# Kernel tuning notes

Hardware: AMD Instinct MI355X
Metric: run time of the kernel (lower is better)

Reference implementation:

```python
import jax, jax.numpy as jnp
import numpy as np

N_NODES = 100000
N_EDGES = 3200000
NEG_SLOPE = 0.2  # PyG GATConv default


def _gat_conv(x, src, dst, W, a_src, a_dst, b, num_nodes):
    # x: [N, Fin]; src/dst: [E'] (self-loops already appended)
    h = x @ W                                   # [N, Fout]
    alpha_src = h @ a_src                       # [N]
    alpha_dst = h @ a_dst                       # [N]
    e = jax.nn.leaky_relu(alpha_src[src] + alpha_dst[dst], NEG_SLOPE)  # [E']
    # segment softmax over incoming edges of each destination node
    e_max = jax.ops.segment_max(e, dst, num_segments=num_nodes)
    e_exp = jnp.exp(e - e_max[dst])
    denom = jax.ops.segment_sum(e_exp, dst, num_segments=num_nodes)
    alpha = e_exp / (denom[dst] + 1e-16)        # [E']
    out = jax.ops.segment_sum(h[src] * alpha[:, None], dst, num_segments=num_nodes)
    return out + b


def setup_inputs() -> dict:
    key = jax.random.key(0)
    ks = jax.random.split(key, 10)
    x = jax.random.normal(ks[0], (N_NODES, 1), jnp.float32)
    edge_index = jax.random.randint(ks[1], (2, N_EDGES), 0, N_NODES, dtype=jnp.int64)
    s1 = 1.0  # glorot-ish scales
    return {
        "x": x,
        "edge_index": edge_index,
        "W1": jax.random.normal(ks[2], (1, 20), jnp.float32) * s1,
        "a_src1": jax.random.normal(ks[3], (20,), jnp.float32) * 0.3,
        "a_dst1": jax.random.normal(ks[4], (20,), jnp.float32) * 0.3,
        "b1": jnp.zeros((20,), jnp.float32),
        "W2": jax.random.normal(ks[5], (20, 20), jnp.float32) * (1.0 / np.sqrt(20.0)),
        "a_src2": jax.random.normal(ks[6], (20,), jnp.float32) * 0.3,
        "a_dst2": jax.random.normal(ks[7], (20,), jnp.float32) * 0.3,
        "b2": jnp.zeros((20,), jnp.float32),
        "Wl": jax.random.normal(ks[8], (20, 1), jnp.float32) * (1.0 / np.sqrt(20.0)),
        "bl": jnp.zeros((1,), jnp.float32),
    }


def reference(x, edge_index, W1, a_src1, a_dst1, b1, W2, a_src2, a_dst2, b2, Wl, bl):
    n = x.shape[0]
    loop = jnp.arange(n, dtype=edge_index.dtype)
    src = jnp.concatenate([edge_index[0], loop])  # add_self_loops=True
    dst = jnp.concatenate([edge_index[1], loop])
    h = _gat_conv(x, src, dst, W1, a_src1, a_dst1, b1, n)
    h = jax.nn.relu(h)
    h = _gat_conv(h, src, dst, W2, a_src2, a_dst2, b2, n)
    h = jax.nn.relu(h)
    return h @ Wl + bl  # [N, 1]
```

## Files before the change

### kernel.cpp

```cpp
#include <hip/hip_runtime.h>
#include <hip/hip_fp16.h>

#define FDIM 20
#define NSLOPE 0.2f
#define BSHIFT 7
#define BSIZE 128
#define BCAP 4800
#define MAXBUCK 800
#define PGRID 512
#define HSTRIDE 32
#define ABLK 512
#define ITMAX 7
#define CHCAP 6272
#define OFFSTRIDE 132

__device__ __forceinline__ float lrelu(float v) { return v > 0.f ? v : NSLOPE * v; }

__global__ void __launch_bounds__(1024)
k_part(const int* __restrict__ ei, int E, int nbuck,
       const float* __restrict__ x, const float* __restrict__ W1,
       const float* __restrict__ a_src, const float* __restrict__ a_dst,
       float2* __restrict__ PX, float* __restrict__ AD,
       int* __restrict__ gcur, int* __restrict__ slab, int N)
{
    __shared__ int hist[MAXBUCK];
    __shared__ int lofs[MAXBUCK];
    __shared__ int gbase[MAXBUCK];
    __shared__ int sbuf[CHCAP];
    __shared__ unsigned short sbk[CHCAP];
    const int tid = threadIdx.x;

    {
        int g = blockIdx.x * 1024 + tid;
        if (g < N) {
            float cs = 0.f, cd = 0.f;
#pragma unroll
            for (int f = 0; f < FDIM; ++f) {
                float w = W1[f]; cs += w * a_src[f]; cd += w * a_dst[f];
            }
            float xv = x[g];
            PX[g] = make_float2(xv * cs, xv);
            AD[g] = xv * cd;
        }
    }

    const int chunk = (E + PGRID - 1) / PGRID;
    const int c0 = blockIdx.x * chunk;
    const int c1 = min(c0 + chunk, E);
    for (int t = tid; t < nbuck; t += 1024) hist[t] = 0;
    __syncthreads();

    int ent[ITMAX], meta[ITMAX];
#pragma unroll
    for (int it = 0; it < ITMAX; ++it) {
        int i = c0 + tid + (it << 10);
        meta[it] = -1;
        if (i < c1) {
            int s = ei[i], d = ei[E + i];
            int b = d >> BSHIFT;
            int lp = atomicAdd(&hist[b], 1);
            ent[it]  = (s << BSHIFT) | (d & (BSIZE - 1));
            meta[it] = (lp << 10) | b;
        }
    }
    __syncthreads();

    int myc = 0;
    if (tid < nbuck) {
        myc = hist[tid];
        lofs[tid] = myc;
        gbase[tid] = myc ? atomicAdd(gcur + tid, myc) : 0;
    }
    __syncthreads();
    for (int o = 1; o < nbuck; o <<= 1) {
        int v = 0;
        if (tid < nbuck && tid >= o) v = lofs[tid - o];
        __syncthreads();
        if (tid < nbuck && tid >= o) lofs[tid] += v;
        __syncthreads();
    }
    if (tid < nbuck) lofs[tid] -= myc;
    __syncthreads();

#pragma unroll
    for (int it = 0; it < ITMAX; ++it) {
        int m = meta[it];
        if (m >= 0) {
            int b  = m & 1023;
            int lp = m >> 10;
            int pos = lofs[b] + lp;
            sbuf[pos] = ent[it];
            sbk[pos]  = (unsigned short)b;
        }
    }
    __syncthreads();

    const int cnt = c1 - c0;
    for (int i = tid; i < cnt; i += 1024) {
        int b  = sbk[i];
        int gp = gbase[b] + (i - lofs[b]);
        if (gp < BCAP) slab[(size_t)b * BCAP + gp] = sbuf[i];
    }
}

__device__ __forceinline__ void sort_bucket(const int* __restrict__ sp, int cnt,
                                            int* __restrict__ sedge,
                                            int* __restrict__ off,
                                            int* __restrict__ cur)
{
    const int tid = threadIdx.x;
    if (tid < BSIZE + 1) off[tid] = 0;
    __syncthreads();
    for (int i = tid; i < cnt; i += ABLK)
        atomicAdd(&off[(sp[i] & (BSIZE - 1)) + 1], 1);
    __syncthreads();
    if (tid < 64) {
        int a = off[2 * tid + 1];
        int c = off[2 * tid + 2];
        int s = a + c;
#pragma unroll
        for (int o = 1; o < 64; o <<= 1) {
            int t = __shfl_up(s, o);
            if (tid >= o) s += t;
        }
        int ex = s - a - c;
        off[2 * tid]     = ex;
        off[2 * tid + 1] = ex + a;
        cur[2 * tid]     = ex;
        cur[2 * tid + 1] = ex + a;
        if (tid == 63) off[BSIZE] = s;
    }
    __syncthreads();
    for (int i = tid; i < cnt; i += ABLK) {
        int e = sp[i];
        int pos = atomicAdd(&cur[e & (BSIZE - 1)], 1);
        sedge[pos] = e >> BSHIFT;
    }
    __syncthreads();
}

__global__ void __launch_bounds__(ABLK)
k_agg1(const int* __restrict__ gcur, const int* __restrict__ slab,
       const float2* __restrict__ PX, const float* __restrict__ AD,
       const float* __restrict__ W1, const float* __restrict__ b1,
       const float* __restrict__ W2,
       const float* __restrict__ as2w, const float* __restrict__ ad2w,
       __half* __restrict__ H, float* __restrict__ AD2,
       int* __restrict__ sedge_g, int* __restrict__ off_g, int N)
{
    __shared__ int sedge[BCAP];
    __shared__ int off[BSIZE + 1], cur[BSIZE];
    __shared__ float sAD[BSIZE];
    __shared__ float sW1[FDIM], sb1[FDIM], sW2[FDIM * FDIM], sas[FDIM], sad[FDIM];
    const int tid = threadIdx.x;
    const int b = blockIdx.x;
    const int dbase = b << BSHIFT;
    if (tid < BSIZE) { int d = dbase + tid; sAD[tid] = (d < N) ? AD[d] : 0.f; }
    for (int t = tid; t < FDIM * FDIM; t += ABLK) sW2[t] = W2[t];
    if (tid >= 480 && tid < 480 + FDIM) {
        int k = tid - 480;
        sW1[k] = W1[k]; sb1[k] = b1[k]; sas[k] = as2w[k]; sad[k] = ad2w[k];
    }
    const int cnt = min(gcur[b], BCAP);
    sort_bucket(slab + (size_t)b * BCAP, cnt, sedge, off, cur);

    for (int i = tid; i < cnt; i += ABLK) sedge_g[(size_t)b * BCAP + i] = sedge[i];
    if (tid <= BSIZE) off_g[b * OFFSTRIDE + tid] = off[tid];

    const int dl = tid >> 2, sub = tid & 3;
    const float adv = sAD[dl];
    float den = 0.f, sx = 0.f;
    const int e1 = off[dl + 1];
#pragma unroll 2
    for (int j = off[dl] + sub; j < e1; j += 4) {
        int s = sedge[j];
        float2 p = PX[s];
        float w = __expf(lrelu(p.x + adv));
        den += w; sx += w * p.y;
    }
    den += __shfl_xor(den, 1); den += __shfl_xor(den, 2);
    sx  += __shfl_xor(sx, 1);  sx  += __shfl_xor(sx, 2);
    const int d = dbase + dl;
    if (sub == 0 && d < N) {
        float2 p = PX[d];
        float w = __expf(lrelu(p.x + adv));
        den += w; sx += w * p.y;
        float sv = sx / (den + 1e-16f);
        float tk[FDIM];
#pragma unroll
        for (int k = 0; k < FDIM; ++k) {
            float tv = sv * sW1[k] + sb1[k];
            tk[k] = tv > 0.f ? tv : 0.f;
        }
        float pas = 0.f, pad = 0.f;
        __half2* hrow = (__half2*)(H + (size_t)d * HSTRIDE);
#pragma unroll
        for (int f = 0; f < FDIM; f += 2) {
            float h0 = 0.f, h1 = 0.f;
#pragma unroll
            for (int k = 0; k < FDIM; ++k) {
                h0 += tk[k] * sW2[k * FDIM + f];
                h1 += tk[k] * sW2[k * FDIM + f + 1];
            }
            hrow[f >> 1] = __halves2half2(__float2half(h0), __float2half(h1));
            pas += h0 * sas[f] + h1 * sas[f + 1];
            pad += h0 * sad[f] + h1 * sad[f + 1];
        }
        *(float*)(H + (size_t)d * HSTRIDE + 24) = pas;
        AD2[d] = pad;
    }
}

__global__ void __launch_bounds__(ABLK)
k_agg2(const int* __restrict__ gcur, const int* __restrict__ sedge_g,
       const int* __restrict__ off_g,
       const __half* __restrict__ H, const float* __restrict__ AD2,
       const float* __restrict__ b2, const float* __restrict__ Wl,
       const float* __restrict__ bl,
       float* __restrict__ out, int N)
{
    __shared__ int sedge[BCAP];
    __shared__ int off[BSIZE + 1];
    __shared__ float sAD[BSIZE];
    __shared__ float sb2[FDIM], sWl[FDIM];
    const int tid = threadIdx.x;
    const int b = blockIdx.x;
    const int dbase = b << BSHIFT;
    if (tid < BSIZE) { int d = dbase + tid; sAD[tid] = (d < N) ? AD2[d] : 0.f; }
    if (tid >= 480 && tid < 480 + FDIM) {
        int k = tid - 480;
        sb2[k] = b2[k]; sWl[k] = Wl[k];
    }
    const int cnt = min(gcur[b], BCAP);
    for (int i = tid; i < cnt; i += ABLK) sedge[i] = sedge_g[(size_t)b * BCAP + i];
    if (tid <= BSIZE) off[tid] = off_g[b * OFFSTRIDE + tid];
    __syncthreads();

    const int dl = tid >> 2, sub = tid & 3;
    const int lane3 = (tid & 63) | 3;
    const float adv = sAD[dl];
    float den = 0.f;
    float acc[8];
#pragma unroll
    for (int t = 0; t < 8; ++t) acc[t] = 0.f;
    const int e1 = off[dl + 1];
#pragma unroll 2
    for (int j = off[dl]; j < e1; ++j) {
        int s = sedge[j];
        uint4 q = ((const uint4*)(H + (size_t)s * HSTRIDE))[sub];
        float al = __shfl(__uint_as_float(q.x), lane3);
        float w = __expf(lrelu(al + adv));
        den += w;
        float2 f;
        f = __half22float2(*(__half2*)&q.x); acc[0] += w * f.x; acc[1] += w * f.y;
        f = __half22float2(*(__half2*)&q.y); acc[2] += w * f.x; acc[3] += w * f.y;
        f = __half22float2(*(__half2*)&q.z); acc[4] += w * f.x; acc[5] += w * f.y;
        f = __half22float2(*(__half2*)&q.w); acc[6] += w * f.x; acc[7] += w * f.y;
    }

    const int d = dbase + dl;
    float r = 0.f;
    if (d < N) {
        uint4 q = ((const uint4*)(H + (size_t)d * HSTRIDE))[sub];
        float al = __shfl(__uint_as_float(q.x), lane3);
        float w = __expf(lrelu(al + adv));
        den += w;
        float hv[8];
        float2 f;
        f = __half22float2(*(__half2*)&q.x); hv[0] = f.x; hv[1] = f.y;
        f = __half22float2(*(__half2*)&q.y); hv[2] = f.x; hv[3] = f.y;
        f = __half22float2(*(__half2*)&q.z); hv[4] = f.x; hv[5] = f.y;
        f = __half22float2(*(__half2*)&q.w); hv[6] = f.x; hv[7] = f.y;
        float inv = 1.f / (den + 1e-16f);
        const int base = sub << 3;
        const int nf = (sub < 2) ? 8 : (sub == 2 ? 4 : 0);
#pragma unroll
        for (int t = 0; t < 8; ++t) {
            if (t < nf) {
                float v = (acc[t] + w * hv[t]) * inv + sb2[base + t];
                v = v > 0.f ? v : 0.f;
                r += v * sWl[base + t];
            }
        }
    }
    r += __shfl_xor(r, 1);
    r += __shfl_xor(r, 2);
    if (sub == 0 && d < N) out[d] = r + bl[0];
}

extern "C" void kernel_launch(void* const* d_in, const int* in_sizes, int n_in,
                              void* d_out, int out_size, void* d_ws, size_t ws_size,
                              hipStream_t stream)
{
    const float* x      = (const float*)d_in[0];
    const int*   ei     = (const int*)d_in[1];
    const float* W1     = (const float*)d_in[2];
    const float* a_src1 = (const float*)d_in[3];
    const float* a_dst1 = (const float*)d_in[4];
    const float* b1     = (const float*)d_in[5];
    const float* W2     = (const float*)d_in[6];
    const float* a_src2 = (const float*)d_in[7];
    const float* a_dst2 = (const float*)d_in[8];
    const float* b2     = (const float*)d_in[9];
    const float* Wl     = (const float*)d_in[10];
    const float* bl     = (const float*)d_in[11];
    float* out = (float*)d_out;

    const int N = in_sizes[0];
    const int E = in_sizes[1] / 2;
    const int NBUCK = (N + BSIZE - 1) >> BSHIFT;

    __half* H    = (__half*)d_ws;
    float2* PX   = (float2*)(H + (size_t)N * HSTRIDE);
    float*  AD   = (float*)(PX + N);
    float*  AD2  = AD + N;
    int*  gcur   = (int*)(AD2 + N);
    int*  slab   = gcur + MAXBUCK;
    int*  sedge_g = slab + (size_t)MAXBUCK * BCAP;
    int*  off_g   = sedge_g + (size_t)MAXBUCK * BCAP;

    hipMemsetAsync(gcur, 0, MAXBUCK * sizeof(int), stream);
    k_part<<<PGRID, 1024, 0, stream>>>(ei, E, NBUCK, x, W1, a_src1, a_dst1,
                                       PX, AD, gcur, slab, N);
    k_agg1<<<NBUCK, ABLK, 0, stream>>>(gcur, slab, PX, AD, W1, b1, W2,
                                       a_src2, a_dst2, H, AD2, sedge_g, off_g, N);
    k_agg2<<<NBUCK, ABLK, 0, stream>>>(gcur, sedge_g, off_g, H, AD2, b2, Wl, bl, out, N);
}
```

Measured before the change: 183.8 us.

## Split agg2 edges across sub-lanes and spread layer-2 transform across four lanes

In the second aggregation kernel, each of the four lanes per destination now handles a quarter of the edges and loads the full 48-byte H row. Before, all four lanes walked every edge and each read its own 16-byte slice. Partial sums for the 20 features and the denominator are then reduced with shuffles. In the first aggregation kernel, the per-node 20x20 W2 transform and the H row store are now split over the four sub-lanes, which were idle before. The first-layer edge loop unroll is also raised to 4. The trade-off is more registers (20 accumulators) and more shuffle reductions, in exchange for fewer serial edge iterations per lane.

```diff
diff --git a/kernel.cpp b/kernel.cpp
--- a/kernel.cpp
+++ b/kernel.cpp
@@ -171,7 +171,7 @@
     const float adv = sAD[dl];
     float den = 0.f, sx = 0.f;
     const int e1 = off[dl + 1];
-#pragma unroll 2
+#pragma unroll 4
     for (int j = off[dl] + sub; j < e1; j += 4) {
         int s = sedge[j];
         float2 p = PX[s];
@@ -181,7 +181,7 @@
     den += __shfl_xor(den, 1); den += __shfl_xor(den, 2);
     sx  += __shfl_xor(sx, 1);  sx  += __shfl_xor(sx, 2);
     const int d = dbase + dl;
-    if (sub == 0 && d < N) {
+    if (d < N) {
         float2 p = PX[d];
         float w = __expf(lrelu(p.x + adv));
         den += w; sx += w * p.y;
@@ -192,22 +192,34 @@
             float tv = sv * sW1[k] + sb1[k];
             tk[k] = tv > 0.f ? tv : 0.f;
         }
+        const int fbase = sub << 3;
+        const int nf = (sub < 2) ? 8 : (sub == 2 ? 4 : 0);
+        float hv[8];
         float pas = 0.f, pad = 0.f;
-        __half2* hrow = (__half2*)(H + (size_t)d * HSTRIDE);
-#pragma unroll
-        for (int f = 0; f < FDIM; f += 2) {
-            float h0 = 0.f, h1 = 0.f;
-#pragma unroll
-            for (int k = 0; k < FDIM; ++k) {
-                h0 += tk[k] * sW2[k * FDIM + f];
-                h1 += tk[k] * sW2[k * FDIM + f + 1];
+#pragma unroll
+        for (int t = 0; t < 8; ++t) {
+            float hsum = 0.f;
+            if (t < nf) {
+#pragma unroll
+                for (int k = 0; k < FDIM; ++k)
+                    hsum += tk[k] * sW2[k * FDIM + fbase + t];
+                pas += hsum * sas[fbase + t];
+                pad += hsum * sad[fbase + t];
             }
-            hrow[f >> 1] = __halves2half2(__float2half(h0), __float2half(h1));
-            pas += h0 * sas[f] + h1 * sas[f + 1];
-            pad += h0 * sad[f] + h1 * sad[f + 1];
-        }
-        *(float*)(H + (size_t)d * HSTRIDE + 24) = pas;
-        AD2[d] = pad;
+            hv[t] = hsum;
+        }
+        pas += __shfl_xor(pas, 1); pas += __shfl_xor(pas, 2);
+        pad += __shfl_xor(pad, 1); pad += __shfl_xor(pad, 2);
+        __half2 p01 = __halves2half2(__float2half(hv[0]), __float2half(hv[1]));
+        __half2 p23 = __halves2half2(__float2half(hv[2]), __float2half(hv[3]));
+        __half2 p45 = __halves2half2(__float2half(hv[4]), __float2half(hv[5]));
+        __half2 p67 = __halves2half2(__float2half(hv[6]), __float2half(hv[7]));
+        uint4 q;
+        q.x = *(unsigned*)&p01; q.y = *(unsigned*)&p23;
+        q.z = *(unsigned*)&p45; q.w = *(unsigned*)&p67;
+        if (sub == 2) { q.z = __float_as_uint(pas); q.w = 0u; }
+        if (sub < 3) ((uint4*)(H + (size_t)d * HSTRIDE))[sub] = q;
+        else AD2[d] = pad;
     }
 }
 
@@ -237,55 +249,67 @@
     __syncthreads();
 
     const int dl = tid >> 2, sub = tid & 3;
-    const int lane3 = (tid & 63) | 3;
     const float adv = sAD[dl];
     float den = 0.f;
-    float acc[8];
-#pragma unroll
-    for (int t = 0; t < 8; ++t) acc[t] = 0.f;
+    float acc[FDIM];
+#pragma unroll
+    for (int k = 0; k < FDIM; ++k) acc[k] = 0.f;
     const int e1 = off[dl + 1];
-#pragma unroll 2
-    for (int j = off[dl]; j < e1; ++j) {
+#pragma unroll 4
+    for (int j = off[dl] + sub; j < e1; j += 4) {
         int s = sedge[j];
-        uint4 q = ((const uint4*)(H + (size_t)s * HSTRIDE))[sub];
-        float al = __shfl(__uint_as_float(q.x), lane3);
-        float w = __expf(lrelu(al + adv));
+        const uint4* rp = (const uint4*)(H + (size_t)s * HSTRIDE);
+        uint4 a = rp[0];
+        uint4 bb = rp[1];
+        uint4 c = rp[2];
+        float w = __expf(lrelu(__uint_as_float(c.z) + adv));
         den += w;
         float2 f;
-        f = __half22float2(*(__half2*)&q.x); acc[0] += w * f.x; acc[1] += w * f.y;
-        f = __half22float2(*(__half2*)&q.y); acc[2] += w * f.x; acc[3] += w * f.y;
-        f = __half22float2(*(__half2*)&q.z); acc[4] += w * f.x; acc[5] += w * f.y;
-        f = __half22float2(*(__half2*)&q.w); acc[6] += w * f.x; acc[7] += w * f.y;
-    }
-
+        f = __half22float2(*(__half2*)&a.x);  acc[0]  += w * f.x; acc[1]  += w * f.y;
+        f = __half22float2(*(__half2*)&a.y);  acc[2]  += w * f.x; acc[3]  += w * f.y;
+        f = __half22float2(*(__half2*)&a.z);  acc[4]  += w * f.x; acc[5]  += w * f.y;
+        f = __half22float2(*(__half2*)&a.w);  acc[6]  += w * f.x; acc[7]  += w * f.y;
+        f = __half22float2(*(__half2*)&bb.x); acc[8]  += w * f.x; acc[9]  += w * f.y;
+        f = __half22float2(*(__half2*)&bb.y); acc[10] += w * f.x; acc[11] += w * f.y;
+        f = __half22float2(*(__half2*)&bb.z); acc[12] += w * f.x; acc[13] += w * f.y;
+        f = __half22float2(*(__half2*)&bb.w); acc[14] += w * f.x; acc[15] += w * f.y;
+        f = __half22float2(*(__half2*)&c.x);  acc[16] += w * f.x; acc[17] += w * f.y;
+        f = __half22float2(*(__half2*)&c.y);  acc[18] += w * f.x; acc[19] += w * f.y;
+    }
+    den += __shfl_xor(den, 1); den += __shfl_xor(den, 2);
+#pragma unroll
+    for (int k = 0; k < FDIM; ++k) {
+        acc[k] += __shfl_xor(acc[k], 1);
+        acc[k] += __shfl_xor(acc[k], 2);
+    }
     const int d = dbase + dl;
-    float r = 0.f;
-    if (d < N) {
-        uint4 q = ((const uint4*)(H + (size_t)d * HSTRIDE))[sub];
-        float al = __shfl(__uint_as_float(q.x), lane3);
-        float w = __expf(lrelu(al + adv));
+    if (sub == 0 && d < N) {
+        const uint4* rp = (const uint4*)(H + (size_t)d * HSTRIDE);
+        uint4 a = rp[0], bb = rp[1], c = rp[2];
+        float w = __expf(lrelu(__uint_as_float(c.z) + adv));
         den += w;
-        float hv[8];
+        float hv[FDIM];
         float2 f;
-        f = __half22float2(*(__half2*)&q.x); hv[0] = f.x; hv[1] = f.y;
-        f = __half22float2(*(__half2*)&q.y); hv[2] = f.x; hv[3] = f.y;
-        f = __half22float2(*(__half2*)&q.z); hv[4] = f.x; hv[5] = f.y;
-        f = __half22float2(*(__half2*)&q.w); hv[6] = f.x; hv[7] = f.y;
+        f = __half22float2(*(__half2*)&a.x);  hv[0]  = f.x; hv[1]  = f.y;
+        f = __half22float2(*(__half2*)&a.y);  hv[2]  = f.x; hv[3]  = f.y;
+        f = __half22float2(*(__half2*)&a.z);  hv[4]  = f.x; hv[5]  = f.y;
+        f = __half22float2(*(__half2*)&a.w);  hv[6]  = f.x; hv[7]  = f.y;
+        f = __half22float2(*(__half2*)&bb.x); hv[8]  = f.x; hv[9]  = f.y;
+        f = __half22float2(*(__half2*)&bb.y); hv[10] = f.x; hv[11] = f.y;
+        f = __half22float2(*(__half2*)&bb.z); hv[12] = f.x; hv[13] = f.y;
+        f = __half22float2(*(__half2*)&bb.w); hv[14] = f.x; hv[15] = f.y;
+        f = __half22float2(*(__half2*)&c.x);  hv[16] = f.x; hv[17] = f.y;
+        f = __half22float2(*(__half2*)&c.y);  hv[18] = f.x; hv[19] = f.y;
         float inv = 1.f / (den + 1e-16f);
-        const int base = sub << 3;
-        const int nf = (sub < 2) ? 8 : (sub == 2 ? 4 : 0);
-#pragma unroll
-        for (int t = 0; t < 8; ++t) {
-            if (t < nf) {
-                float v = (acc[t] + w * hv[t]) * inv + sb2[base + t];
-                v = v > 0.f ? v : 0.f;
-                r += v * sWl[base + t];
-            }
-        }
-    }
-    r += __shfl_xor(r, 1);
-    r += __shfl_xor(r, 2);
-    if (sub == 0 && d < N) out[d] = r + bl[0];
+        float r = 0.f;
+#pragma unroll
+        for (int k = 0; k < FDIM; ++k) {
+            float v = (acc[k] + w * hv[k]) * inv + sb2[k];
+            v = v > 0.f ? v : 0.f;
+            r += v * sWl[k];
+        }
+        out[d] = r + bl[0];
+    }
 }
 
 extern "C" void kernel_launch(void* const* d_in, const int* in_sizes, int n_in,
```

New measurement: 176.6 us. -3.9%, faster.
